# Performance work log

Hardware: AMD Instinct MI355X
Metric: run time of the kernel (lower is better)

## Reference

```python
import jax, jax.numpy as jnp
import numpy as np

HEAD_SIZE = 64

def setup_inputs() -> dict:
    key = jax.random.key(0)
    k1, k2, k3 = jax.random.split(key, 3)
    B, T, C = 4, 4096, 1024
    x = jax.random.normal(k1, (B, T, C), dtype=jnp.float32)
    # nn.Linear(C, head_size, bias=False); stored as [in, out] so x @ W matches x @ weight.T
    Wk = jax.random.normal(k2, (C, HEAD_SIZE), dtype=jnp.float32) * (C ** -0.5)
    Wv = jax.random.normal(k3, (C, HEAD_SIZE), dtype=jnp.float32) * (C ** -0.5)
    return {"x": x, "Wk": Wk, "Wv": Wv}

def reference(x, Wk, Wv):
    # Faithful to source: q = self.key(x)  (query projection is unused -> Q == K)
    B, T, C = x.shape
    k = jnp.einsum('btc,ch->bth', x, Wk)           # [B,T,H]
    q = jnp.einsum('btc,ch->bth', x, Wk)           # same projection (source bug)
    scores = jnp.einsum('bth,bsh->bts', q, k) * (HEAD_SIZE ** -0.5)  # [B,T,T]
    causal = jnp.tril(jnp.ones((T, T), dtype=bool))
    scores = jnp.where(causal, scores, -jnp.inf)
    weights = jax.nn.softmax(scores, axis=-1)      # dropout p=0 (eval) -> identity
    v = jnp.einsum('btc,ch->bth', x, Wv)
    out = jnp.einsum('bts,bsh->bth', weights, v)   # [B,T,H]
    return out
```

## Files before the change

kernel.cpp:

```cpp
#include <hip/hip_runtime.h>

typedef short bf16x8 __attribute__((ext_vector_type(8)));
typedef float f32x4 __attribute__((ext_vector_type(4)));
typedef float f32x16 __attribute__((ext_vector_type(16)));
typedef unsigned u32x4v __attribute__((ext_vector_type(4)));

#define T_SEQ 4096
#define CDIM  1024
#define HD    64
#define NROWS 16384

__device__ inline float exp2fast(float x) {
  return __builtin_amdgcn_exp2f(x);
}

__device__ inline unsigned short f2bf(float f) {
  unsigned u = __builtin_bit_cast(unsigned, f);
  u = (u + 0x7fffu + ((u >> 16) & 1u)) >> 16;
  return (unsigned short)u;
}
__device__ inline unsigned cvt_pk_bf16(float lo, float hi) {
  unsigned r;
  asm("v_cvt_pk_bf16_f32 %0, %1, %2" : "=v"(r) : "v"(lo), "v"(hi));
  return r;
}
__device__ inline float bf2f(unsigned short u) {
  unsigned v = (unsigned)u << 16;
  return __builtin_bit_cast(float, v);
}

__global__ __launch_bounds__(256) void prep_w(
    const float* __restrict__ Wk, const float* __restrict__ Wv,
    unsigned short* __restrict__ Wt) {
  int n = blockIdx.x;
  const float* W = (n < 64) ? Wk : Wv;
  int col = n & 63;
  for (int k = threadIdx.x; k < CDIM; k += 256)
    Wt[(size_t)n * CDIM + k] = f2bf(W[(size_t)k * HD + col]);
}

__global__ __launch_bounds__(256) void proj_mfma(
    const float* __restrict__ x, const unsigned short* __restrict__ Wt,
    unsigned short* __restrict__ Kb, unsigned short* __restrict__ Vb) {
  __shared__ __align__(16) unsigned char xsb[16384];
  __shared__ __align__(16) unsigned char wsb[32768];
  const int tid = threadIdx.x;
  const int lane = tid & 63, wave = tid >> 6;
  const int wm = wave & 1, wn = wave >> 1;
  const int lg = lane >> 4, lc = lane & 15;
  const int row0 = blockIdx.x * 64;

  float4 xreg[8];
  uint4 wreg[8];
  auto load_tiles = [&](int kk) {
    #pragma unroll
    for (int p = 0; p < 8; ++p) {
      int idx = tid + 256 * p, r = idx >> 5, c4 = idx & 31;
      xreg[p] = *(const float4*)&x[(size_t)(row0 + r) * CDIM + kk + c4 * 4];
    }
    #pragma unroll
    for (int p = 0; p < 8; ++p) {
      int idx = tid + 256 * p, r = idx >> 4, c8 = idx & 15;
      wreg[p] = *(const uint4*)&Wt[(size_t)r * CDIM + kk + c8 * 8];
    }
  };
  auto write_tiles = [&]() {
    #pragma unroll
    for (int p = 0; p < 8; ++p) {
      int idx = tid + 256 * p, r = idx >> 5, c4 = idx & 31;
      uint2 v;
      v.x = cvt_pk_bf16(xreg[p].x, xreg[p].y);
      v.y = cvt_pk_bf16(xreg[p].z, xreg[p].w);
      int byt = (r * 256 + c4 * 8) ^ ((r & 7) << 4);
      *(uint2*)(xsb + byt) = v;
    }
    #pragma unroll
    for (int p = 0; p < 8; ++p) {
      int idx = tid + 256 * p, r = idx >> 4, c8 = idx & 15;
      int byt = (r * 256 + c8 * 16) ^ ((r & 7) << 4);
      *(uint4*)(wsb + byt) = wreg[p];
    }
  };

  f32x4 acc[2][4];
  #pragma unroll
  for (int mf = 0; mf < 2; ++mf)
    #pragma unroll
    for (int nf = 0; nf < 4; ++nf) acc[mf][nf] = (f32x4){0.f, 0.f, 0.f, 0.f};

  load_tiles(0);
  for (int kk = 0; kk < CDIM; kk += 128) {
    __syncthreads();
    write_tiles();
    __syncthreads();
    if (kk + 128 < CDIM) load_tiles(kk + 128);
    #pragma unroll
    for (int dd = 0; dd < 4; ++dd) {
      bf16x8 a[2], bfr[4];
      #pragma unroll
      for (int mf = 0; mf < 2; ++mf) {
        int r = wm * 32 + mf * 16 + lc;
        int sw = (r & 7) << 4;
        a[mf] = *(const bf16x8*)(xsb + ((r * 256 + dd * 64 + lg * 16) ^ sw));
      }
      #pragma unroll
      for (int nf = 0; nf < 4; ++nf) {
        int r = wn * 64 + nf * 16 + lc;
        int sw = (r & 7) << 4;
        bfr[nf] = *(const bf16x8*)(wsb + ((r * 256 + dd * 64 + lg * 16) ^ sw));
      }
      __builtin_amdgcn_s_setprio(1);
      #pragma unroll
      for (int mf = 0; mf < 2; ++mf)
        #pragma unroll
        for (int nf = 0; nf < 4; ++nf)
          acc[mf][nf] = __builtin_amdgcn_mfma_f32_16x16x32_bf16(a[mf], bfr[nf], acc[mf][nf], 0, 0, 0);
      __builtin_amdgcn_s_setprio(0);
    }
  }

  unsigned short* Ob = (wn == 0) ? Kb : Vb;
  #pragma unroll
  for (int mf = 0; mf < 2; ++mf)
    #pragma unroll
    for (int r = 0; r < 4; ++r) {
      int rg = row0 + wm * 32 + mf * 16 + lg * 4 + r;
      #pragma unroll
      for (int nf = 0; nf < 4; ++nf)
        Ob[(size_t)rg * HD + nf * 16 + lc] = f2bf(acc[mf][nf][r]);
    }
}

__global__ __launch_bounds__(256) void attn_part(
    const unsigned short* __restrict__ Kb, const unsigned short* __restrict__ Vb,
    unsigned short* __restrict__ Opart, float* __restrict__ Ml) {
  __shared__ __align__(16) unsigned char lds[32768];

  const int tid = threadIdx.x;
  const int lane = tid & 63;
  const int wq = tid >> 6;
  const int hi = lane >> 5;
  const int lq = lane & 31;

  const int b = blockIdx.x & 3;
  int qb = 0, c = 0;
  {
    int u = blockIdx.x >> 2, acc = 0;
    for (int q = 31; q >= 0; --q) {
      int nch = (q + 2) >> 1;
      if (u < acc + nch) { qb = q; c = u - acc; break; }
      acc += nch;
    }
  }
  const int kstart = c * 256;
  const int kend = min(kstart + 256, (qb + 1) * 128);
  const int nit = (kend - kstart) >> 6;
  const int q0g = qb * 128 + wq * 32;
  const int qg = q0g + lq;
  const size_t base = (size_t)b * T_SEQ;
  const float SCALE2 = 0.18033688011112042f;

  bf16x8 qf[4];
  {
    const unsigned short* qp = &Kb[(base + q0g + lq) * HD];
    #pragma unroll
    for (int dd = 0; dd < 4; ++dd) {
      bf16x8 t = *(const bf16x8*)&qp[dd * 16 + hi * 8];
      const unsigned short* ts = (const unsigned short*)&t;
      unsigned ow[4];
      #pragma unroll
      for (int w = 0; w < 4; ++w)
        ow[w] = cvt_pk_bf16(bf2f(ts[2 * w]) * SCALE2, bf2f(ts[2 * w + 1]) * SCALE2);
      u32x4v ov = {ow[0], ow[1], ow[2], ow[3]};
      qf[dd] = __builtin_bit_cast(bf16x8, ov);
    }
  }

  f32x16 oT0, oT1;
  #pragma unroll
  for (int r = 0; r < 16; ++r) { oT0[r] = 0.f; oT1[r] = 0.f; }
  float mreg = -1e30f, lreg = 0.f;

  uint4 kreg[2], vreg0, vreg1;
  auto load_kv = [&](int jj) {
    const size_t kv0 = (base + kstart + (size_t)jj * 64) * HD;
    #pragma unroll
    for (int p = 0; p < 2; ++p) {
      int idx = tid + 256 * p, r = idx >> 3, c8 = idx & 7;
      kreg[p] = *(const uint4*)&Kb[kv0 + (size_t)r * HD + c8 * 8];
    }
    int key0 = (tid & 31) * 2, d0 = (tid >> 5) * 8;
    vreg0 = *(const uint4*)&Vb[kv0 + (size_t)key0 * HD + d0];
    vreg1 = *(const uint4*)&Vb[kv0 + (size_t)(key0 + 1) * HD + d0];
  };
  auto write_kv = [&](int buf) {
    unsigned char* kb = lds + buf * 16384;
    unsigned char* vb = kb + 8192;
    #pragma unroll
    for (int p = 0; p < 2; ++p) {
      int idx = tid + 256 * p, r = idx >> 3, c8 = idx & 7;
      int byt = (r * 128 + c8 * 16) ^ ((r & 7) << 4);
      *(uint4*)(kb + byt) = kreg[p];
    }
    int key0 = (tid & 31) * 2, d0 = (tid >> 5) * 8;
    const unsigned short* pa = (const unsigned short*)&vreg0;
    const unsigned short* pb = (const unsigned short*)&vreg1;
    #pragma unroll
    for (int j = 0; j < 8; ++j) {
      unsigned val = (unsigned)pa[j] | ((unsigned)pb[j] << 16);
      int d = d0 + j;
      int byt = (d * 128 + key0 * 2) ^ ((d & 7) << 4);
      *(unsigned*)(vb + byt) = val;
    }
  };

  auto qk = [&](int buf, int ksub) -> f32x16 {
    const unsigned char* kb = lds + buf * 16384;
    f32x16 sacc;
    #pragma unroll
    for (int r = 0; r < 16; ++r) sacc[r] = 0.f;
    const int krow = ksub * 32 + lq;
    const int ksw = (krow & 7) << 4;
    #pragma unroll
    for (int dd = 0; dd < 4; ++dd) {
      bf16x8 kf = *(const bf16x8*)(kb + ((krow * 128 + dd * 32 + hi * 16) ^ ksw));
      sacc = __builtin_amdgcn_mfma_f32_32x32x16_bf16(kf, qf[dd], sacc, 0, 0, 0);
    }
    return sacc;
  };
  auto maskdiag = [&](f32x16& s, int kbase_s) {
    #pragma unroll
    for (int r = 0; r < 16; ++r) {
      int key = kbase_s + (r & 3) + 8 * (r >> 2) + 4 * hi;
      if (key > qg) s[r] = -1e38f;
    }
  };
  auto max16 = [&](const f32x16& s) -> float {
    return fmaxf(
        fmaxf(fmaxf(fmaxf(s[0], s[1]), fmaxf(s[2], s[3])),
              fmaxf(fmaxf(s[4], s[5]), fmaxf(s[6], s[7]))),
        fmaxf(fmaxf(fmaxf(s[8], s[9]), fmaxf(s[10], s[11])),
              fmaxf(fmaxf(s[12], s[13]), fmaxf(s[14], s[15]))));
  };
  auto pack2 = [&](const f32x16& s, bf16x8& p1, bf16x8& p2) {
    unsigned pk[8];
    #pragma unroll
    for (int i = 0; i < 8; ++i) pk[i] = cvt_pk_bf16(s[2 * i], s[2 * i + 1]);
    unsigned wA[4], wB[4];
    #pragma unroll
    for (int i = 0; i < 2; ++i) {
      unsigned a0 = pk[i], b0 = pk[2 + i];
      unsigned sa = (unsigned)__shfl_xor((int)a0, 32);
      unsigned sb = (unsigned)__shfl_xor((int)b0, 32);
      wA[i] = hi ? sb : a0;
      wA[2 + i] = hi ? b0 : sa;
      unsigned c0 = pk[4 + i], d0v = pk[6 + i];
      unsigned sc = (unsigned)__shfl_xor((int)c0, 32);
      unsigned sd = (unsigned)__shfl_xor((int)d0v, 32);
      wB[i] = hi ? sd : c0;
      wB[2 + i] = hi ? d0v : sc;
    }
    u32x4v t1v = {wA[0], wA[1], wA[2], wA[3]};
    u32x4v t2v = {wB[0], wB[1], wB[2], wB[3]};
    p1 = __builtin_bit_cast(bf16x8, t1v);
    p2 = __builtin_bit_cast(bf16x8, t2v);
  };
  auto pv = [&](int buf, int ksub, bf16x8 pb1, bf16x8 pb2) {
    const unsigned char* vb = lds + buf * 16384 + 8192;
    const int cb = ksub * 64;
    {
      int drow = lq;
      int swz = (drow & 7) << 4;
      bf16x8 v0 = *(const bf16x8*)(vb + ((drow * 128 + cb + hi * 16) ^ swz));
      bf16x8 v1 = *(const bf16x8*)(vb + ((drow * 128 + cb + 32 + hi * 16) ^ swz));
      oT0 = __builtin_amdgcn_mfma_f32_32x32x16_bf16(v0, pb1, oT0, 0, 0, 0);
      oT0 = __builtin_amdgcn_mfma_f32_32x32x16_bf16(v1, pb2, oT0, 0, 0, 0);
    }
    {
      int drow = 32 + lq;
      int swz = (drow & 7) << 4;
      bf16x8 v0 = *(const bf16x8*)(vb + ((drow * 128 + cb + hi * 16) ^ swz));
      bf16x8 v1 = *(const bf16x8*)(vb + ((drow * 128 + cb + 32 + hi * 16) ^ swz));
      oT1 = __builtin_amdgcn_mfma_f32_32x32x16_bf16(v0, pb1, oT1, 0, 0, 0);
      oT1 = __builtin_amdgcn_mfma_f32_32x32x16_bf16(v1, pb2, oT1, 0, 0, 0);
    }
  };

  load_kv(0);
  write_kv(0);
  for (int jj = 0; jj < nit; ++jj) {
    const int cur = jj & 1;
    __syncthreads();
    if (jj + 1 < nit) load_kv(jj + 1);
    const int kb0 = kstart + jj * 64;

    if (kb0 + 32 <= q0g) {
      __builtin_amdgcn_s_setprio(1);
      f32x16 s0 = qk(cur, 0);
      f32x16 s1 = qk(cur, 1);
      __builtin_amdgcn_s_setprio(0);
      if (kb0 + 32 == q0g) maskdiag(s1, kb0 + 32);
      float mx = fmaxf(max16(s0), max16(s1));
      mx = fmaxf(mx, __shfl_xor(mx, 32));
      if (!__all(mx <= mreg + 11.5f)) {
        float mn = fmaxf(mreg, mx);
        float al = exp2fast(mreg - mn);
        lreg *= al;
        #pragma unroll
        for (int r = 0; r < 16; ++r) { oT0[r] *= al; oT1[r] *= al; }
        mreg = mn;
      }
      float ps = 0.f;
      #pragma unroll
      for (int r = 0; r < 16; ++r) {
        float p0 = exp2fast(s0[r] - mreg);
        float p1 = exp2fast(s1[r] - mreg);
        ps += p0 + p1;
        s0[r] = p0;
        s1[r] = p1;
      }
      lreg += ps + __shfl_xor(ps, 32);
      bf16x8 pa1, pa2, pbb1, pbb2;
      pack2(s0, pa1, pa2);
      pack2(s1, pbb1, pbb2);
      __builtin_amdgcn_s_setprio(1);
      pv(cur, 0, pa1, pa2);
      pv(cur, 1, pbb1, pbb2);
      __builtin_amdgcn_s_setprio(0);
    } else if (kb0 <= q0g) {
      __builtin_amdgcn_s_setprio(1);
      f32x16 s0 = qk(cur, 0);
      __builtin_amdgcn_s_setprio(0);
      if (kb0 == q0g) maskdiag(s0, kb0);
      float mx = max16(s0);
      mx = fmaxf(mx, __shfl_xor(mx, 32));
      if (!__all(mx <= mreg + 11.5f)) {
        float mn = fmaxf(mreg, mx);
        float al = exp2fast(mreg - mn);
        lreg *= al;
        #pragma unroll
        for (int r = 0; r < 16; ++r) { oT0[r] *= al; oT1[r] *= al; }
        mreg = mn;
      }
      float ps = 0.f;
      #pragma unroll
      for (int r = 0; r < 16; ++r) {
        float p = exp2fast(s0[r] - mreg);
        ps += p;
        s0[r] = p;
      }
      lreg += ps + __shfl_xor(ps, 32);
      bf16x8 pa1, pa2;
      pack2(s0, pa1, pa2);
      __builtin_amdgcn_s_setprio(1);
      pv(cur, 0, pa1, pa2);
      __builtin_amdgcn_s_setprio(0);
    }

    if (jj + 1 < nit) write_kv(cur ^ 1);
  }

  unsigned short* op = Opart + (size_t)blockIdx.x * 8192;
  const float invl = 1.0f / lreg;
  const int qrow = wq * 32 + lq;
  #pragma unroll
  for (int g = 0; g < 4; ++g) {
    int d0 = 8 * g + 4 * hi;
    uint2 w0, w1;
    w0.x = cvt_pk_bf16(oT0[4 * g] * invl, oT0[4 * g + 1] * invl);
    w0.y = cvt_pk_bf16(oT0[4 * g + 2] * invl, oT0[4 * g + 3] * invl);
    w1.x = cvt_pk_bf16(oT1[4 * g] * invl, oT1[4 * g + 1] * invl);
    w1.y = cvt_pk_bf16(oT1[4 * g + 2] * invl, oT1[4 * g + 3] * invl);
    *(uint2*)&op[qrow * 64 + d0] = w0;
    *(uint2*)&op[qrow * 64 + d0 + 32] = w1;
  }
  if (hi == 0) {
    Ml[(size_t)blockIdx.x * 256 + qrow * 2] = mreg;
    Ml[(size_t)blockIdx.x * 256 + qrow * 2 + 1] = lreg;
  }
}

__global__ __launch_bounds__(256) void attn_merge(
    const unsigned short* __restrict__ Opart, const float* __restrict__ Ml,
    float* __restrict__ out) {
  int g = blockIdx.x * 256 + threadIdx.x;
  int d8 = (g & 7) * 8;
  int q128 = (g >> 3) & 127;
  int qb = (g >> 10) & 31;
  int b = (g >> 15) & 3;
  int nch = (qb + 2) >> 1;
  int us = 0;
  for (int q = 31; q > qb; --q) us += (q + 2) >> 1;
  float M = -1e30f;
  for (int cc = 0; cc < nch; ++cc) {
    int part = (us + cc) * 4 + b;
    M = fmaxf(M, Ml[(size_t)part * 256 + q128 * 2]);
  }
  float L = 0.f;
  float o[8];
  #pragma unroll
  for (int j = 0; j < 8; ++j) o[j] = 0.f;
  for (int cc = 0; cc < nch; ++cc) {
    int part = (us + cc) * 4 + b;
    float mc = Ml[(size_t)part * 256 + q128 * 2];
    float lc = Ml[(size_t)part * 256 + q128 * 2 + 1];
    float w = exp2fast(mc - M) * lc;
    L += w;
    uint4 v = *(const uint4*)&Opart[(size_t)part * 8192 + q128 * 64 + d8];
    const unsigned short* pv = (const unsigned short*)&v;
    #pragma unroll
    for (int j = 0; j < 8; ++j) o[j] += w * bf2f(pv[j]);
  }
  float inv = 1.0f / L;
  size_t og = ((size_t)b * T_SEQ + qb * 128 + q128) * 64 + d8;
  float4 r0 = make_float4(o[0] * inv, o[1] * inv, o[2] * inv, o[3] * inv);
  float4 r1 = make_float4(o[4] * inv, o[5] * inv, o[6] * inv, o[7] * inv);
  *(float4*)&out[og] = r0;
  *(float4*)&out[og + 4] = r1;
}

extern "C" void kernel_launch(void* const* d_in, const int* in_sizes, int n_in,
                              void* d_out, int out_size, void* d_ws, size_t ws_size,
                              hipStream_t stream) {
  const float* x  = (const float*)d_in[0];
  const float* Wk = (const float*)d_in[1];
  const float* Wv = (const float*)d_in[2];
  unsigned short* Kb = (unsigned short*)d_ws;
  unsigned short* Vb = Kb + (size_t)NROWS * HD;
  unsigned short* Wt = Vb + (size_t)NROWS * HD;
  unsigned short* Opart = Wt + (size_t)128 * CDIM;
  float* Ml = (float*)(Opart + (size_t)1088 * 8192);
  float* o = (float*)d_out;

  prep_w<<<128, 256, 0, stream>>>(Wk, Wv, Wt);
  proj_mfma<<<256, 256, 0, stream>>>(x, Wt, Kb, Vb);
  attn_part<<<1088, 256, 0, stream>>>(Kb, Vb, Opart, Ml);
  attn_merge<<<512, 256, 0, stream>>>(Opart, Ml, o);
}
```

Before: 85.32 us.

## Double query rows per wave to reuse each K/V tile across 64 queries

The attention kernel now gives each block 256 query rows, with each wave owning two 32-row query groups, instead of 128 rows. Each K tile loaded from LDS then feeds MFMAs for both query groups, which halves the block count and the K/V global and LDS traffic per query. The cost is higher register pressure from four output accumulators and two softmax states, which may lower occupancy. Fewer blocks on the GPU may also leave the causal load less balanced. The merge kernel and workspace layout are updated to match.

```diff
diff --git a/kernel.cpp b/kernel.cpp
--- a/kernel.cpp
+++ b/kernel.cpp
@@ -127,7 +127,7 @@
       int rg = row0 + wm * 32 + mf * 16 + lg * 4 + r;
       #pragma unroll
       for (int nf = 0; nf < 4; ++nf)
-        Ob[(size_t)rg * HD + nf * 16 + lc] = f2bf(acc[mf][nf][r]);
+        Ob[(size_t)rg * HD + nf * 16 + lc] = f2bf(acc[nf == 0 ? mf : mf][nf][r]);
     }
 }
 
@@ -143,43 +143,49 @@
   const int lq = lane & 31;
 
   const int b = blockIdx.x & 3;
-  int qb = 0, c = 0;
+  int qp = 0, c = 0;
   {
     int u = blockIdx.x >> 2, acc = 0;
-    for (int q = 31; q >= 0; --q) {
-      int nch = (q + 2) >> 1;
-      if (u < acc + nch) { qb = q; c = u - acc; break; }
+    for (int q = 15; q >= 0; --q) {
+      int nch = q + 1;
+      if (u < acc + nch) { qp = q; c = u - acc; break; }
       acc += nch;
     }
   }
   const int kstart = c * 256;
-  const int kend = min(kstart + 256, (qb + 1) * 128);
-  const int nit = (kend - kstart) >> 6;
-  const int q0g = qb * 128 + wq * 32;
-  const int qg = q0g + lq;
+  const int q0g = qp * 256 + wq * 64;
+  const int qgA = q0g + lq;
+  const int qgB = q0g + 32 + lq;
   const size_t base = (size_t)b * T_SEQ;
   const float SCALE2 = 0.18033688011112042f;
 
-  bf16x8 qf[4];
+  bf16x8 qfA[4], qfB[4];
   {
-    const unsigned short* qp = &Kb[(base + q0g + lq) * HD];
+    const unsigned short* qpA = &Kb[(base + q0g + lq) * HD];
+    const unsigned short* qpB = &Kb[(base + q0g + 32 + lq) * HD];
     #pragma unroll
     for (int dd = 0; dd < 4; ++dd) {
-      bf16x8 t = *(const bf16x8*)&qp[dd * 16 + hi * 8];
-      const unsigned short* ts = (const unsigned short*)&t;
-      unsigned ow[4];
-      #pragma unroll
-      for (int w = 0; w < 4; ++w)
-        ow[w] = cvt_pk_bf16(bf2f(ts[2 * w]) * SCALE2, bf2f(ts[2 * w + 1]) * SCALE2);
-      u32x4v ov = {ow[0], ow[1], ow[2], ow[3]};
-      qf[dd] = __builtin_bit_cast(bf16x8, ov);
-    }
-  }
-
-  f32x16 oT0, oT1;
+      bf16x8 tA = *(const bf16x8*)&qpA[dd * 16 + hi * 8];
+      bf16x8 tB = *(const bf16x8*)&qpB[dd * 16 + hi * 8];
+      const unsigned short* tsA = (const unsigned short*)&tA;
+      const unsigned short* tsB = (const unsigned short*)&tB;
+      unsigned owA[4], owB[4];
+      #pragma unroll
+      for (int w = 0; w < 4; ++w) {
+        owA[w] = cvt_pk_bf16(bf2f(tsA[2 * w]) * SCALE2, bf2f(tsA[2 * w + 1]) * SCALE2);
+        owB[w] = cvt_pk_bf16(bf2f(tsB[2 * w]) * SCALE2, bf2f(tsB[2 * w + 1]) * SCALE2);
+      }
+      u32x4v ovA = {owA[0], owA[1], owA[2], owA[3]};
+      u32x4v ovB = {owB[0], owB[1], owB[2], owB[3]};
+      qfA[dd] = __builtin_bit_cast(bf16x8, ovA);
+      qfB[dd] = __builtin_bit_cast(bf16x8, ovB);
+    }
+  }
+
+  f32x16 oA0, oA1, oB0, oB1;
   #pragma unroll
-  for (int r = 0; r < 16; ++r) { oT0[r] = 0.f; oT1[r] = 0.f; }
-  float mreg = -1e30f, lreg = 0.f;
+  for (int r = 0; r < 16; ++r) { oA0[r] = 0.f; oA1[r] = 0.f; oB0[r] = 0.f; oB1[r] = 0.f; }
+  float mA = -1e30f, lA = 0.f, mB = -1e30f, lB = 0.f;
 
   uint4 kreg[2], vreg0, vreg1;
   auto load_kv = [&](int jj) {
@@ -214,27 +220,6 @@
     }
   };
 
-  auto qk = [&](int buf, int ksub) -> f32x16 {
-    const unsigned char* kb = lds + buf * 16384;
-    f32x16 sacc;
-    #pragma unroll
-    for (int r = 0; r < 16; ++r) sacc[r] = 0.f;
-    const int krow = ksub * 32 + lq;
-    const int ksw = (krow & 7) << 4;
-    #pragma unroll
-    for (int dd = 0; dd < 4; ++dd) {
-      bf16x8 kf = *(const bf16x8*)(kb + ((krow * 128 + dd * 32 + hi * 16) ^ ksw));
-      sacc = __builtin_amdgcn_mfma_f32_32x32x16_bf16(kf, qf[dd], sacc, 0, 0, 0);
-    }
-    return sacc;
-  };
-  auto maskdiag = [&](f32x16& s, int kbase_s) {
-    #pragma unroll
-    for (int r = 0; r < 16; ++r) {
-      int key = kbase_s + (r & 3) + 8 * (r >> 2) + 4 * hi;
-      if (key > qg) s[r] = -1e38f;
-    }
-  };
   auto max16 = [&](const f32x16& s) -> float {
     return fmaxf(
         fmaxf(fmaxf(fmaxf(s[0], s[1]), fmaxf(s[2], s[3])),
@@ -246,137 +231,141 @@
     unsigned pk[8];
     #pragma unroll
     for (int i = 0; i < 8; ++i) pk[i] = cvt_pk_bf16(s[2 * i], s[2 * i + 1]);
-    unsigned wA[4], wB[4];
+    unsigned wA_[4], wB_[4];
     #pragma unroll
     for (int i = 0; i < 2; ++i) {
       unsigned a0 = pk[i], b0 = pk[2 + i];
       unsigned sa = (unsigned)__shfl_xor((int)a0, 32);
       unsigned sb = (unsigned)__shfl_xor((int)b0, 32);
-      wA[i] = hi ? sb : a0;
-      wA[2 + i] = hi ? b0 : sa;
+      wA_[i] = hi ? sb : a0;
+      wA_[2 + i] = hi ? b0 : sa;
       unsigned c0 = pk[4 + i], d0v = pk[6 + i];
       unsigned sc = (unsigned)__shfl_xor((int)c0, 32);
       unsigned sd = (unsigned)__shfl_xor((int)d0v, 32);
-      wB[i] = hi ? sd : c0;
-      wB[2 + i] = hi ? d0v : sc;
-    }
-    u32x4v t1v = {wA[0], wA[1], wA[2], wA[3]};
-    u32x4v t2v = {wB[0], wB[1], wB[2], wB[3]};
+      wB_[i] = hi ? sd : c0;
+      wB_[2 + i] = hi ? d0v : sc;
+    }
+    u32x4v t1v = {wA_[0], wA_[1], wA_[2], wA_[3]};
+    u32x4v t2v = {wB_[0], wB_[1], wB_[2], wB_[3]};
     p1 = __builtin_bit_cast(bf16x8, t1v);
     p2 = __builtin_bit_cast(bf16x8, t2v);
   };
-  auto pv = [&](int buf, int ksub, bf16x8 pb1, bf16x8 pb2) {
+  auto smpv = [&](f32x16& s, float& m, float& l, f32x16& o0, f32x16& o1,
+                  bool domask, int kbase_s, int qg_t, int buf, int ksub) {
+    if (domask) {
+      #pragma unroll
+      for (int r = 0; r < 16; ++r) {
+        int key = kbase_s + (r & 3) + 8 * (r >> 2) + 4 * hi;
+        if (key > qg_t) s[r] = -1e38f;
+      }
+    }
+    float mx = max16(s);
+    mx = fmaxf(mx, __shfl_xor(mx, 32));
+    if (!__all(mx <= m + 11.5f)) {
+      float mn = fmaxf(m, mx);
+      float al = exp2fast(m - mn);
+      l *= al;
+      #pragma unroll
+      for (int r = 0; r < 16; ++r) { o0[r] *= al; o1[r] *= al; }
+      m = mn;
+    }
+    float ps = 0.f;
+    #pragma unroll
+    for (int r = 0; r < 16; ++r) {
+      float p = exp2fast(s[r] - m);
+      ps += p;
+      s[r] = p;
+    }
+    l += ps + __shfl_xor(ps, 32);
+    bf16x8 p1, p2;
+    pack2(s, p1, p2);
     const unsigned char* vb = lds + buf * 16384 + 8192;
     const int cb = ksub * 64;
+    __builtin_amdgcn_s_setprio(1);
     {
       int drow = lq;
       int swz = (drow & 7) << 4;
       bf16x8 v0 = *(const bf16x8*)(vb + ((drow * 128 + cb + hi * 16) ^ swz));
       bf16x8 v1 = *(const bf16x8*)(vb + ((drow * 128 + cb + 32 + hi * 16) ^ swz));
-      oT0 = __builtin_amdgcn_mfma_f32_32x32x16_bf16(v0, pb1, oT0, 0, 0, 0);
-      oT0 = __builtin_amdgcn_mfma_f32_32x32x16_bf16(v1, pb2, oT0, 0, 0, 0);
+      o0 = __builtin_amdgcn_mfma_f32_32x32x16_bf16(v0, p1, o0, 0, 0, 0);
+      o0 = __builtin_amdgcn_mfma_f32_32x32x16_bf16(v1, p2, o0, 0, 0, 0);
     }
     {
       int drow = 32 + lq;
       int swz = (drow & 7) << 4;
       bf16x8 v0 = *(const bf16x8*)(vb + ((drow * 128 + cb + hi * 16) ^ swz));
       bf16x8 v1 = *(const bf16x8*)(vb + ((drow * 128 + cb + 32 + hi * 16) ^ swz));
-      oT1 = __builtin_amdgcn_mfma_f32_32x32x16_bf16(v0, pb1, oT1, 0, 0, 0);
-      oT1 = __builtin_amdgcn_mfma_f32_32x32x16_bf16(v1, pb2, oT1, 0, 0, 0);
-    }
+      o1 = __builtin_amdgcn_mfma_f32_32x32x16_bf16(v0, p1, o1, 0, 0, 0);
+      o1 = __builtin_amdgcn_mfma_f32_32x32x16_bf16(v1, p2, o1, 0, 0, 0);
+    }
+    __builtin_amdgcn_s_setprio(0);
   };
 
   load_kv(0);
   write_kv(0);
-  for (int jj = 0; jj < nit; ++jj) {
+  for (int jj = 0; jj < 4; ++jj) {
     const int cur = jj & 1;
     __syncthreads();
-    if (jj + 1 < nit) load_kv(jj + 1);
+    if (jj + 1 < 4) load_kv(jj + 1);
     const int kb0 = kstart + jj * 64;
 
-    if (kb0 + 32 <= q0g) {
+    #pragma unroll
+    for (int ksub = 0; ksub < 2; ++ksub) {
+      const int kbase_s = kb0 + ksub * 32;
+      if (kbase_s > q0g + 32) continue;
+      const unsigned char* kb = lds + cur * 16384;
+      const int krow = ksub * 32 + lq;
+      const int ksw = (krow & 7) << 4;
+      bf16x8 kf[4];
+      #pragma unroll
+      for (int dd = 0; dd < 4; ++dd)
+        kf[dd] = *(const bf16x8*)(kb + ((krow * 128 + dd * 32 + hi * 16) ^ ksw));
+      const bool doA = kbase_s <= q0g;
+      f32x16 sA, sB;
+      #pragma unroll
+      for (int r = 0; r < 16; ++r) { sA[r] = 0.f; sB[r] = 0.f; }
       __builtin_amdgcn_s_setprio(1);
-      f32x16 s0 = qk(cur, 0);
-      f32x16 s1 = qk(cur, 1);
+      #pragma unroll
+      for (int dd = 0; dd < 4; ++dd) {
+        sB = __builtin_amdgcn_mfma_f32_32x32x16_bf16(kf[dd], qfB[dd], sB, 0, 0, 0);
+        if (doA) sA = __builtin_amdgcn_mfma_f32_32x32x16_bf16(kf[dd], qfA[dd], sA, 0, 0, 0);
+      }
       __builtin_amdgcn_s_setprio(0);
-      if (kb0 + 32 == q0g) maskdiag(s1, kb0 + 32);
-      float mx = fmaxf(max16(s0), max16(s1));
-      mx = fmaxf(mx, __shfl_xor(mx, 32));
-      if (!__all(mx <= mreg + 11.5f)) {
-        float mn = fmaxf(mreg, mx);
-        float al = exp2fast(mreg - mn);
-        lreg *= al;
-        #pragma unroll
-        for (int r = 0; r < 16; ++r) { oT0[r] *= al; oT1[r] *= al; }
-        mreg = mn;
-      }
-      float ps = 0.f;
-      #pragma unroll
-      for (int r = 0; r < 16; ++r) {
-        float p0 = exp2fast(s0[r] - mreg);
-        float p1 = exp2fast(s1[r] - mreg);
-        ps += p0 + p1;
-        s0[r] = p0;
-        s1[r] = p1;
-      }
-      lreg += ps + __shfl_xor(ps, 32);
-      bf16x8 pa1, pa2, pbb1, pbb2;
-      pack2(s0, pa1, pa2);
-      pack2(s1, pbb1, pbb2);
-      __builtin_amdgcn_s_setprio(1);
-      pv(cur, 0, pa1, pa2);
-      pv(cur, 1, pbb1, pbb2);
-      __builtin_amdgcn_s_setprio(0);
-    } else if (kb0 <= q0g) {
-      __builtin_amdgcn_s_setprio(1);
-      f32x16 s0 = qk(cur, 0);
-      __builtin_amdgcn_s_setprio(0);
-      if (kb0 == q0g) maskdiag(s0, kb0);
-      float mx = max16(s0);
-      mx = fmaxf(mx, __shfl_xor(mx, 32));
-      if (!__all(mx <= mreg + 11.5f)) {
-        float mn = fmaxf(mreg, mx);
-        float al = exp2fast(mreg - mn);
-        lreg *= al;
-        #pragma unroll
-        for (int r = 0; r < 16; ++r) { oT0[r] *= al; oT1[r] *= al; }
-        mreg = mn;
-      }
-      float ps = 0.f;
-      #pragma unroll
-      for (int r = 0; r < 16; ++r) {
-        float p = exp2fast(s0[r] - mreg);
-        ps += p;
-        s0[r] = p;
-      }
-      lreg += ps + __shfl_xor(ps, 32);
-      bf16x8 pa1, pa2;
-      pack2(s0, pa1, pa2);
-      __builtin_amdgcn_s_setprio(1);
-      pv(cur, 0, pa1, pa2);
-      __builtin_amdgcn_s_setprio(0);
-    }
-
-    if (jj + 1 < nit) write_kv(cur ^ 1);
-  }
-
-  unsigned short* op = Opart + (size_t)blockIdx.x * 8192;
-  const float invl = 1.0f / lreg;
-  const int qrow = wq * 32 + lq;
+      if (doA) smpv(sA, mA, lA, oA0, oA1, kbase_s == q0g, kbase_s, qgA, cur, ksub);
+      smpv(sB, mB, lB, oB0, oB1, kbase_s == q0g + 32, kbase_s, qgB, cur, ksub);
+    }
+
+    if (jj + 1 < 4) write_kv(cur ^ 1);
+  }
+
+  unsigned short* op = Opart + (size_t)blockIdx.x * 16384;
+  float* mlp = Ml + (size_t)blockIdx.x * 512;
+  const float invA = 1.0f / lA;
+  const float invB = 1.0f / lB;
+  const int rowA = wq * 64 + lq;
+  const int rowB = wq * 64 + 32 + lq;
   #pragma unroll
   for (int g = 0; g < 4; ++g) {
     int d0 = 8 * g + 4 * hi;
-    uint2 w0, w1;
-    w0.x = cvt_pk_bf16(oT0[4 * g] * invl, oT0[4 * g + 1] * invl);
-    w0.y = cvt_pk_bf16(oT0[4 * g + 2] * invl, oT0[4 * g + 3] * invl);
-    w1.x = cvt_pk_bf16(oT1[4 * g] * invl, oT1[4 * g + 1] * invl);
-    w1.y = cvt_pk_bf16(oT1[4 * g + 2] * invl, oT1[4 * g + 3] * invl);
-    *(uint2*)&op[qrow * 64 + d0] = w0;
-    *(uint2*)&op[qrow * 64 + d0 + 32] = w1;
+    uint2 wa0, wa1, wb0, wb1;
+    wa0.x = cvt_pk_bf16(oA0[4 * g] * invA, oA0[4 * g + 1] * invA);
+    wa0.y = cvt_pk_bf16(oA0[4 * g + 2] * invA, oA0[4 * g + 3] * invA);
+    wa1.x = cvt_pk_bf16(oA1[4 * g] * invA, oA1[4 * g + 1] * invA);
+    wa1.y = cvt_pk_bf16(oA1[4 * g + 2] * invA, oA1[4 * g + 3] * invA);
+    wb0.x = cvt_pk_bf16(oB0[4 * g] * invB, oB0[4 * g + 1] * invB);
+    wb0.y = cvt_pk_bf16(oB0[4 * g + 2] * invB, oB0[4 * g + 3] * invB);
+    wb1.x = cvt_pk_bf16(oB1[4 * g] * invB, oB1[4 * g + 1] * invB);
+    wb1.y = cvt_pk_bf16(oB1[4 * g + 2] * invB, oB1[4 * g + 3] * invB);
+    *(uint2*)&op[rowA * 64 + d0] = wa0;
+    *(uint2*)&op[rowA * 64 + d0 + 32] = wa1;
+    *(uint2*)&op[rowB * 64 + d0] = wb0;
+    *(uint2*)&op[rowB * 64 + d0 + 32] = wb1;
   }
   if (hi == 0) {
-    Ml[(size_t)blockIdx.x * 256 + qrow * 2] = mreg;
-    Ml[(size_t)blockIdx.x * 256 + qrow * 2 + 1] = lreg;
+    mlp[rowA * 2] = mA;
+    mlp[rowA * 2 + 1] = lA;
+    mlp[rowB * 2] = mB;
+    mlp[rowB * 2 + 1] = lB;
   }
 }
 
@@ -385,16 +374,18 @@
     float* __restrict__ out) {
   int g = blockIdx.x * 256 + threadIdx.x;
   int d8 = (g & 7) * 8;
-  int q128 = (g >> 3) & 127;
-  int qb = (g >> 10) & 31;
-  int b = (g >> 15) & 3;
-  int nch = (qb + 2) >> 1;
+  int row = g >> 3;
+  int b = row >> 12;
+  int t = row & (T_SEQ - 1);
+  int qp = t >> 8;
+  int r256 = t & 255;
+  int nch = qp + 1;
   int us = 0;
-  for (int q = 31; q > qb; --q) us += (q + 2) >> 1;
+  for (int q = 15; q > qp; --q) us += q + 1;
   float M = -1e30f;
   for (int cc = 0; cc < nch; ++cc) {
     int part = (us + cc) * 4 + b;
-    M = fmaxf(M, Ml[(size_t)part * 256 + q128 * 2]);
+    M = fmaxf(M, Ml[(size_t)part * 512 + r256 * 2]);
   }
   float L = 0.f;
   float o[8];
@@ -402,17 +393,17 @@
   for (int j = 0; j < 8; ++j) o[j] = 0.f;
   for (int cc = 0; cc < nch; ++cc) {
     int part = (us + cc) * 4 + b;
-    float mc = Ml[(size_t)part * 256 + q128 * 2];
-    float lc = Ml[(size_t)part * 256 + q128 * 2 + 1];
+    float mc = Ml[(size_t)part * 512 + r256 * 2];
+    float lc = Ml[(size_t)part * 512 + r256 * 2 + 1];
     float w = exp2fast(mc - M) * lc;
     L += w;
-    uint4 v = *(const uint4*)&Opart[(size_t)part * 8192 + q128 * 64 + d8];
+    uint4 v = *(const uint4*)&Opart[(size_t)part * 16384 + r256 * 64 + d8];
     const unsigned short* pv = (const unsigned short*)&v;
     #pragma unroll
     for (int j = 0; j < 8; ++j) o[j] += w * bf2f(pv[j]);
   }
   float inv = 1.0f / L;
-  size_t og = ((size_t)b * T_SEQ + qb * 128 + q128) * 64 + d8;
+  size_t og = ((size_t)b * T_SEQ + qp * 256 + r256) * 64 + d8;
   float4 r0 = make_float4(o[0] * inv, o[1] * inv, o[2] * inv, o[3] * inv);
   float4 r1 = make_float4(o[4] * inv, o[5] * inv, o[6] * inv, o[7] * inv);
   *(float4*)&out[og] = r0;
@@ -429,11 +420,11 @@
   unsigned short* Vb = Kb + (size_t)NROWS * HD;
   unsigned short* Wt = Vb + (size_t)NROWS * HD;
   unsigned short* Opart = Wt + (size_t)128 * CDIM;
-  float* Ml = (float*)(Opart + (size_t)1088 * 8192);
+  float* Ml = (float*)(Opart + (size_t)544 * 16384);
   float* o = (float*)d_out;
 
   prep_w<<<128, 256, 0, stream>>>(Wk, Wv, Wt);
   proj_mfma<<<256, 256, 0, stream>>>(x, Wt, Kb, Vb);
-  attn_part<<<1088, 256, 0, stream>>>(Kb, Vb, Opart, Ml);
+  attn_part<<<544, 256, 0, stream>>>(Kb, Vb, Opart, Ml);
   attn_merge<<<512, 256, 0, stream>>>(Opart, Ml, o);
 }
```

New measurement: 102.8 us. 20.5% more time.

## Defer PV matmul one iteration with triple-buffered K/V LDS to overlap softmax

Applied to the files above, without the earlier changes.

Enlarges shared memory to three K/V buffers and defers the P·V MFMA of each full tile into the next iteration, issuing it right after that iteration's QK^T MFMAs. The goal is to overlap matrix-core work with the exp/max softmax VALU work of the current tile. It adds register pressure from holding the packed P fragments, uses more LDS (which may cut occupancy), and adds a modulo-3 buffer index.

```diff
diff --git a/kernel.cpp b/kernel.cpp
--- a/kernel.cpp
+++ b/kernel.cpp
@@ -134,7 +134,7 @@
 __global__ __launch_bounds__(256) void attn_part(
     const unsigned short* __restrict__ Kb, const unsigned short* __restrict__ Vb,
     unsigned short* __restrict__ Opart, float* __restrict__ Ml) {
-  __shared__ __align__(16) unsigned char lds[32768];
+  __shared__ __align__(16) unsigned char lds[49152];
 
   const int tid = threadIdx.x;
   const int lane = tid & 63;
@@ -286,10 +286,14 @@
     }
   };
 
+  bool pend = false;
+  int pendBuf = 0;
+  bf16x8 pp0a, pp0b, pp1a, pp1b;
+
   load_kv(0);
   write_kv(0);
   for (int jj = 0; jj < nit; ++jj) {
-    const int cur = jj & 1;
+    const int cur = jj % 3;
     __syncthreads();
     if (jj + 1 < nit) load_kv(jj + 1);
     const int kb0 = kstart + jj * 64;
@@ -298,6 +302,11 @@
       __builtin_amdgcn_s_setprio(1);
       f32x16 s0 = qk(cur, 0);
       f32x16 s1 = qk(cur, 1);
+      if (pend) {
+        pv(pendBuf, 0, pp0a, pp0b);
+        pv(pendBuf, 1, pp1a, pp1b);
+        pend = false;
+      }
       __builtin_amdgcn_s_setprio(0);
       if (kb0 + 32 == q0g) maskdiag(s1, kb0 + 32);
       float mx = fmaxf(max16(s0), max16(s1));
@@ -320,16 +329,18 @@
         s1[r] = p1;
       }
       lreg += ps + __shfl_xor(ps, 32);
-      bf16x8 pa1, pa2, pbb1, pbb2;
-      pack2(s0, pa1, pa2);
-      pack2(s1, pbb1, pbb2);
-      __builtin_amdgcn_s_setprio(1);
-      pv(cur, 0, pa1, pa2);
-      pv(cur, 1, pbb1, pbb2);
-      __builtin_amdgcn_s_setprio(0);
+      pack2(s0, pp0a, pp0b);
+      pack2(s1, pp1a, pp1b);
+      pendBuf = cur;
+      pend = true;
     } else if (kb0 <= q0g) {
       __builtin_amdgcn_s_setprio(1);
       f32x16 s0 = qk(cur, 0);
+      if (pend) {
+        pv(pendBuf, 0, pp0a, pp0b);
+        pv(pendBuf, 1, pp1a, pp1b);
+        pend = false;
+      }
       __builtin_amdgcn_s_setprio(0);
       if (kb0 == q0g) maskdiag(s0, kb0);
       float mx = max16(s0);
@@ -355,9 +366,23 @@
       __builtin_amdgcn_s_setprio(1);
       pv(cur, 0, pa1, pa2);
       __builtin_amdgcn_s_setprio(0);
-    }
-
-    if (jj + 1 < nit) write_kv(cur ^ 1);
+    } else {
+      if (pend) {
+        __builtin_amdgcn_s_setprio(1);
+        pv(pendBuf, 0, pp0a, pp0b);
+        pv(pendBuf, 1, pp1a, pp1b);
+        __builtin_amdgcn_s_setprio(0);
+        pend = false;
+      }
+    }
+
+    if (jj + 1 < nit) write_kv((jj + 1) % 3);
+  }
+  if (pend) {
+    __builtin_amdgcn_s_setprio(1);
+    pv(pendBuf, 0, pp0a, pp0b);
+    pv(pendBuf, 1, pp1a, pp1b);
+    __builtin_amdgcn_s_setprio(0);
   }
 
   unsigned short* op = Opart + (size_t)blockIdx.x * 8192;
```

After: 85.64 us. Within noise of the previous version (+0.4%).

## Load W tiles via global_load_lds double-buffering and coalesce weight transpose

Applied to the files above, without the earlier changes.

The projection kernel now copies the bf16 weight tiles straight from global memory into a double-buffered LDS region with global_load_lds, with the XOR swizzle applied on the source address. This drops the register staging and LDS write for W and overlaps the next tile's load with compute. prep_w is rewritten as a tiled transpose through shared memory with coalesced float4 reads and 16-byte bf16 writes. In exchange, LDS use per block doubles to 64KB for W, which may lower occupancy.

```diff
diff --git a/kernel.cpp b/kernel.cpp
--- a/kernel.cpp
+++ b/kernel.cpp
@@ -28,22 +28,44 @@
   unsigned v = (unsigned)u << 16;
   return __builtin_bit_cast(float, v);
 }
+__device__ inline void gload_lds16(const unsigned short* g, unsigned char* l) {
+  __builtin_amdgcn_global_load_lds(
+      (const __attribute__((address_space(1))) unsigned int*)(const void*)g,
+      (__attribute__((address_space(3))) unsigned int*)(void*)l, 16, 0, 0);
+}
 
 __global__ __launch_bounds__(256) void prep_w(
     const float* __restrict__ Wk, const float* __restrict__ Wv,
     unsigned short* __restrict__ Wt) {
-  int n = blockIdx.x;
-  const float* W = (n < 64) ? Wk : Wv;
-  int col = n & 63;
-  for (int k = threadIdx.x; k < CDIM; k += 256)
-    Wt[(size_t)n * CDIM + k] = f2bf(W[(size_t)k * HD + col]);
+  __shared__ float tile[64][68];
+  const int t = threadIdx.x;
+  const int mat = blockIdx.x & 1;
+  const int k0 = (blockIdx.x >> 1) * 64;
+  const float* W = mat ? Wv : Wk;
+  #pragma unroll
+  for (int pp = 0; pp < 4; ++pp) {
+    int idx = t + 256 * pp, row = idx >> 4, c4 = idx & 15;
+    float4 v = *(const float4*)&W[(size_t)(k0 + row) * HD + c4 * 4];
+    *(float4*)&tile[row][c4 * 4] = v;
+  }
+  __syncthreads();
+  #pragma unroll
+  for (int j = 0; j < 2; ++j) {
+    int n = t & 63, j8 = (t >> 6) + 4 * j;
+    unsigned ow[4];
+    #pragma unroll
+    for (int w = 0; w < 4; ++w)
+      ow[w] = cvt_pk_bf16(tile[j8 * 8 + 2 * w][n], tile[j8 * 8 + 2 * w + 1][n]);
+    u32x4v ov = {ow[0], ow[1], ow[2], ow[3]};
+    *(u32x4v*)&Wt[(size_t)(mat * 64 + n) * CDIM + k0 + j8 * 8] = ov;
+  }
 }
 
 __global__ __launch_bounds__(256) void proj_mfma(
     const float* __restrict__ x, const unsigned short* __restrict__ Wt,
     unsigned short* __restrict__ Kb, unsigned short* __restrict__ Vb) {
   __shared__ __align__(16) unsigned char xsb[16384];
-  __shared__ __align__(16) unsigned char wsb[32768];
+  __shared__ __align__(16) unsigned char wsb[65536];
   const int tid = threadIdx.x;
   const int lane = tid & 63, wave = tid >> 6;
   const int wm = wave & 1, wn = wave >> 1;
@@ -51,20 +73,14 @@
   const int row0 = blockIdx.x * 64;
 
   float4 xreg[8];
-  uint4 wreg[8];
-  auto load_tiles = [&](int kk) {
+  auto load_x = [&](int kk) {
     #pragma unroll
     for (int p = 0; p < 8; ++p) {
       int idx = tid + 256 * p, r = idx >> 5, c4 = idx & 31;
       xreg[p] = *(const float4*)&x[(size_t)(row0 + r) * CDIM + kk + c4 * 4];
     }
-    #pragma unroll
-    for (int p = 0; p < 8; ++p) {
-      int idx = tid + 256 * p, r = idx >> 4, c8 = idx & 15;
-      wreg[p] = *(const uint4*)&Wt[(size_t)r * CDIM + kk + c8 * 8];
-    }
-  };
-  auto write_tiles = [&]() {
+  };
+  auto write_x = [&]() {
     #pragma unroll
     for (int p = 0; p < 8; ++p) {
       int idx = tid + 256 * p, r = idx >> 5, c4 = idx & 31;
@@ -74,11 +90,16 @@
       int byt = (r * 256 + c4 * 8) ^ ((r & 7) << 4);
       *(uint2*)(xsb + byt) = v;
     }
+  };
+  auto gload_W = [&](int kk, int buf) {
+    unsigned char* wb = wsb + buf * 32768;
     #pragma unroll
     for (int p = 0; p < 8; ++p) {
-      int idx = tid + 256 * p, r = idx >> 4, c8 = idx & 15;
-      int byt = (r * 256 + c8 * 16) ^ ((r & 7) << 4);
-      *(uint4*)(wsb + byt) = wreg[p];
+      int ci = p * 256 + tid;
+      int r = ci >> 4;
+      int c8 = (ci & 15) ^ (r & 7);
+      gload_lds16(&Wt[(size_t)r * CDIM + kk + c8 * 8],
+                  wb + (p * 256 + wave * 64) * 16);
     }
   };
 
@@ -88,12 +109,15 @@
     #pragma unroll
     for (int nf = 0; nf < 4; ++nf) acc[mf][nf] = (f32x4){0.f, 0.f, 0.f, 0.f};
 
-  load_tiles(0);
+  gload_W(0, 0);
+  load_x(0);
   for (int kk = 0; kk < CDIM; kk += 128) {
+    const int cur = (kk >> 7) & 1;
     __syncthreads();
-    write_tiles();
+    write_x();
     __syncthreads();
-    if (kk + 128 < CDIM) load_tiles(kk + 128);
+    if (kk + 128 < CDIM) { gload_W(kk + 128, cur ^ 1); load_x(kk + 128); }
+    const unsigned char* wb = wsb + cur * 32768;
     #pragma unroll
     for (int dd = 0; dd < 4; ++dd) {
       bf16x8 a[2], bfr[4];
@@ -107,7 +131,7 @@
       for (int nf = 0; nf < 4; ++nf) {
         int r = wn * 64 + nf * 16 + lc;
         int sw = (r & 7) << 4;
-        bfr[nf] = *(const bf16x8*)(wsb + ((r * 256 + dd * 64 + lg * 16) ^ sw));
+        bfr[nf] = *(const bf16x8*)(wb + ((r * 256 + dd * 64 + lg * 16) ^ sw));
       }
       __builtin_amdgcn_s_setprio(1);
       #pragma unroll
@@ -432,7 +456,7 @@
   float* Ml = (float*)(Opart + (size_t)1088 * 8192);
   float* o = (float*)d_out;
 
-  prep_w<<<128, 256, 0, stream>>>(Wk, Wv, Wt);
+  prep_w<<<32, 256, 0, stream>>>(Wk, Wv, Wt);
   proj_mfma<<<256, 256, 0, stream>>>(x, Wt, Kb, Vb);
   attn_part<<<1088, 256, 0, stream>>>(Kb, Vb, Opart, Ml);
   attn_merge<<<512, 256, 0, stream>>>(Opart, Ml, o);
```

After: 73.56 us. 13.8% less time.
